# Kernel optimization log

Measured on AMD Instinct MI355X. Metric: run time of the kernel, lower is better.

## Reference

```python
import jax, jax.numpy as jnp
import numpy as np

ALPHA = 0.2  # LeakyReLU negative slope
NEG_INF = jnp.float32(-9e15)


def gat_layer(h, mask, W, a, concat):
    """Dense GAT layer (pyGAT style). h: [B,N,Fin], mask: [N,N] bool, W: [Fin,Fout], a: [2*Fout,1]."""
    Wh = h @ W                                   # [B,N,Fout]
    F_out = W.shape[-1]
    e_src = Wh @ a[:F_out]                       # [B,N,1]
    e_dst = Wh @ a[F_out:]                       # [B,N,1]
    e = jax.nn.leaky_relu(e_src + jnp.swapaxes(e_dst, -1, -2), ALPHA)  # [B,N,N]
    att = jnp.where(mask, e, NEG_INF)
    att = jax.nn.softmax(att, axis=-1)
    out = att @ Wh                               # [B,N,Fout]
    return jax.nn.elu(out) if concat else out


def setup_inputs() -> dict:
    key = jax.random.key(0)
    ks = jax.random.split(key, 8)
    B, N, nfeat, nhid, nheads, emb, nclass = 4, 2048, 128, 64, 8, 64, 16
    slices = jax.random.normal(ks[0], (B, N, nfeat), jnp.float32)
    adj = jax.random.randint(ks[1], (N, N), 0, 2, jnp.int32)
    s = 1.0 / float(np.sqrt(nfeat))
    Ws = jax.random.uniform(ks[2], (nheads, nfeat, nhid), jnp.float32, -s, s)
    As = jax.random.uniform(ks[3], (nheads, 2 * nhid, 1), jnp.float32, -s, s)
    W1 = jax.random.uniform(ks[4], (nhid * nheads, emb), jnp.float32, -s, s)
    a1 = jax.random.uniform(ks[5], (2 * emb, 1), jnp.float32, -s, s)
    W2 = jax.random.uniform(ks[6], (emb, nclass), jnp.float32, -s, s)
    a2 = jax.random.uniform(ks[7], (2 * nclass, 1), jnp.float32, -s, s)
    return {"slices": slices, "adj": adj, "Ws": Ws, "As": As,
            "W1": W1, "a1": a1, "W2": W2, "a2": a2}


def reference(slices, adj, Ws, As, W1, a1, W2, a2):
    # Eval mode: dropout = 0 (identity).
    mask = adj > 0                               # [N,N], broadcasts over batch
    # Multi-head GAT with concat=True (ELU inside each head), vectorized over heads.
    heads = jax.vmap(lambda W, a: gat_layer(slices, mask, W, a, True))(Ws, As)  # [H,B,N,nhid]
    H, B, N, nh = heads.shape
    x = jnp.moveaxis(heads, 0, 2).reshape(B, N, H * nh)  # concat along features, head-major
    image_feature = jax.nn.elu(gat_layer(x, mask, W1, a1, False))              # [B,N,emb]
    pre = jax.nn.elu(gat_layer(image_feature, mask, W2, a2, False))            # [B,N,nclass]
    pre = pre[:, 0, :]                                                         # [B,nclass]
    return image_feature, pre
```

## Files before the change

kernel.cpp:

```cpp
#include <hip/hip_runtime.h>
#include <hip/hip_bf16.h>
#include <cstdint>


#define NN 2048

typedef float f32x4 __attribute__((ext_vector_type(4)));
typedef __bf16 bf16x8 __attribute__((ext_vector_type(8)));
typedef _Float16 f16;
typedef _Float16 f16x8 __attribute__((ext_vector_type(8)));

__device__ __forceinline__ void gll16(const void* g, void* l) {
  __builtin_amdgcn_global_load_lds(
      (const __attribute__((address_space(1))) unsigned int*)g,
      (__attribute__((address_space(3))) unsigned int*)l, 16, 0, 0);
}

__global__ __launch_bounds__(256) void prep_k(
    const int* __restrict__ adj, unsigned char* __restrict__ pm,
    const float* __restrict__ Ws, __bf16* __restrict__ WsFh, __bf16* __restrict__ WsFl,
    const float* __restrict__ W1, __bf16* __restrict__ W1Fh, __bf16* __restrict__ W1Fl) {
  const int bx = blockIdx.x, t = threadIdx.x;
  if (bx < 2048) {
    const int i = bx;
#pragma unroll
    for (int jt = 0; jt < 8; ++jt) {
      const int j = jt * 256 + t;
      pm[((long)(j >> 5) << 16) + i * 32 + (j & 31)] =
          adj[(long)i * NN + j] > 0 ? 0xFFu : 0u;
    }
  } else if (bx < 2304) {
    const int idx = (bx - 2048) * 256 + t;
    const int inst = idx >> 13;
    const int rem = idx & 8191;
    const int k = rem >> 6, n = rem & 63;
    const float v = Ws[(long)inst * 8192 + rem];
    const __bf16 vh = (__bf16)v;
    const int pos = ((k >> 5) * 4 + (n >> 4)) * 512 + (((k >> 3) & 3) * 16 + (n & 15)) * 8 + (k & 7);
    WsFh[(long)inst * 8192 + pos] = vh;
    WsFl[(long)inst * 8192 + pos] = (__bf16)(v - (float)vh);
  } else {
    const int idx = (bx - 2304) * 256 + t;
    const int k = idx >> 6, n = idx & 63;
    const float v = W1[idx];
    const __bf16 vh = (__bf16)v;
    const int pos = ((k >> 5) * 4 + (n >> 4)) * 512 + (((k >> 3) & 3) * 16 + (n & 15)) * 8 + (k & 7);
    W1Fh[pos] = vh;
    W1Fl[pos] = (__bf16)(v - (float)vh);
  }
}

struct GemmLd {
  float4 a0, a1;
  bf16x8 bh[4], bl[4];
};

__global__ __launch_bounds__(128) void gemm_mfma_k(
    const float* __restrict__ Aall, const __bf16* __restrict__ WFhi,
    const __bf16* __restrict__ WFlo, const float* __restrict__ avecAll,
    f16* __restrict__ WhBAll, float* __restrict__ Eo, float* __restrict__ Go,
    f16* __restrict__ Fo, f16* __restrict__ Ho, float* __restrict__ pC,
    int K, int KS, long aStrideB) {
  const int p = blockIdx.y;
  const int ks = blockIdx.z;
  const float* A = Aall + (long)(p & 3) * aStrideB;
  const long wfOff = (long)(p >> 2) * K * 64;
  const bf16x8* BhF = (const bf16x8*)(WFhi + wfOff);
  const bf16x8* BlF = (const bf16x8*)(WFlo + wfOff);

  const int t = threadIdx.x, lane = t & 63, wave = t >> 6;
  const int quad = lane >> 4, lm = lane & 15;
  const int i0w = blockIdx.x * 32 + wave * 16;
  const float* Arow = A + (long)(i0w + lm) * K;
  const int kBeg = ks * (K / KS), kEnd = kBeg + K / KS;

  f32x4 acc[4];
#pragma unroll
  for (int nt = 0; nt < 4; ++nt) acc[nt] = (f32x4){0.f, 0.f, 0.f, 0.f};

  auto LOAD = [&](GemmLd& L, int k0) {
    L.a0 = *(const float4*)(Arow + k0 + quad * 8);
    L.a1 = *(const float4*)(Arow + k0 + quad * 8 + 4);
    const int bbase = (k0 >> 5) * 256 + lane;
#pragma unroll
    for (int nt = 0; nt < 4; ++nt) {
      L.bh[nt] = BhF[bbase + nt * 64];
      L.bl[nt] = BlF[bbase + nt * 64];
    }
  };
  auto STEP = [&](const GemmLd& L) {
    const float av8[8] = {L.a0.x, L.a0.y, L.a0.z, L.a0.w, L.a1.x, L.a1.y, L.a1.z, L.a1.w};
    bf16x8 ah, al;
#pragma unroll
    for (int j = 0; j < 8; ++j) {
      const __bf16 h = (__bf16)av8[j];
      ah[j] = h;
      al[j] = (__bf16)(av8[j] - (float)h);
    }
#pragma unroll
    for (int nt = 0; nt < 4; ++nt) {
      acc[nt] = __builtin_amdgcn_mfma_f32_16x16x32_bf16(ah, L.bh[nt], acc[nt], 0, 0, 0);
      acc[nt] = __builtin_amdgcn_mfma_f32_16x16x32_bf16(al, L.bh[nt], acc[nt], 0, 0, 0);
      acc[nt] = __builtin_amdgcn_mfma_f32_16x16x32_bf16(ah, L.bl[nt], acc[nt], 0, 0, 0);
    }
  };

  GemmLd La, Lb;
  LOAD(La, kBeg);
  for (int k0 = kBeg; k0 < kEnd; k0 += 64) {
    LOAD(Lb, k0 + 32);
    STEP(La);
    LOAD(La, (k0 + 64 < kEnd) ? k0 + 64 : kBeg);
    STEP(Lb);
  }

  if (KS > 1) {
    float* pc = pC + ((long)(p * KS + ks) * NN) * 64;
#pragma unroll
    for (int reg = 0; reg < 4; ++reg) {
      const int row = i0w + quad * 4 + reg;
#pragma unroll
      for (int nt = 0; nt < 4; ++nt) pc[(long)row * 64 + nt * 16 + lm] = acc[nt][reg];
    }
    return;
  }

  const float* av = avecAll + (long)(p >> 2) * 128;
  f16* WhB = WhBAll + (long)p * NN * 64;
  float* E = Eo + (long)p * NN;
  float* G = Go + (long)p * NN;
  f16* F = Fo + (long)p * NN;
  f16* Hh = Ho + (long)p * NN;

  float alo[4], ahi[4];
#pragma unroll
  for (int nt = 0; nt < 4; ++nt) {
    alo[nt] = av[nt * 16 + lm];
    ahi[nt] = av[64 + nt * 16 + lm];
  }
#pragma unroll
  for (int reg = 0; reg < 4; ++reg) {
    float es = 0.f, ed = 0.f;
#pragma unroll
    for (int nt = 0; nt < 4; ++nt) {
      es += acc[nt][reg] * alo[nt];
      ed += acc[nt][reg] * ahi[nt];
    }
#pragma unroll
    for (int m = 1; m < 16; m <<= 1) {
      es += __shfl_xor(es, m);
      ed += __shfl_xor(ed, m);
    }
    if (lm == 0) {
      const int r = i0w + quad * 4 + reg;
      E[r] = __expf(es);
      G[r] = __expf(0.2f * es);
      F[r] = (f16)__expf(ed);
      Hh[r] = (f16)__expf(0.2f * ed);
    }
  }

  const int r0 = i0w + quad * 4;
  const long base = ((long)(r0 >> 5) * 4) * 512 + (((r0 >> 3) & 3) * 16 + lm) * 8 + (r0 & 7);
#pragma unroll
  for (int nt = 0; nt < 4; ++nt) {
    union { f16 h[4]; uint2 u; } pk;
#pragma unroll
    for (int q = 0; q < 4; ++q) pk.h[q] = (f16)acc[nt][q];
    *(uint2*)(WhB + base + nt * 512) = pk.u;
  }
}

__global__ __launch_bounds__(256) void gemm_epi_k(
    const float* __restrict__ pC, const float* __restrict__ avec,
    f16* __restrict__ WhBAll, float* __restrict__ Eo, float* __restrict__ Go,
    f16* __restrict__ Fo, f16* __restrict__ Ho, int KS) {
  const int inst = blockIdx.y;
  const int t = threadIdx.x;
  const int row = blockIdx.x * 16 + (t >> 4);
  const int cg = t & 15;
  f32x4 c = (f32x4){0.f, 0.f, 0.f, 0.f};
  for (int ks = 0; ks < KS; ++ks)
    c += *(const f32x4*)(pC + (((long)(inst * KS + ks) * NN) + row) * 64 + cg * 4);
  float es = 0.f, ed = 0.f;
#pragma unroll
  for (int q = 0; q < 4; ++q) {
    const int n = cg * 4 + q;
    es += c[q] * avec[n];
    ed += c[q] * avec[64 + n];
  }
#pragma unroll
  for (int m = 1; m < 16; m <<= 1) {
    es += __shfl_xor(es, m);
    ed += __shfl_xor(ed, m);
  }
  if (cg == 0) {
    Eo[(long)inst * NN + row] = __expf(es);
    Go[(long)inst * NN + row] = __expf(0.2f * es);
    Fo[(long)inst * NN + row] = (f16)__expf(ed);
    Ho[(long)inst * NN + row] = (f16)__expf(0.2f * ed);
  }
  f16* WhB = WhBAll + (long)inst * NN * 64;
#pragma unroll
  for (int q = 0; q < 4; ++q) {
    const int n = cg * 4 + q;
    const int pos = ((row >> 5) * 4 + (n >> 4)) * 512 + (((row >> 3) & 3) * 16 + (n & 15)) * 8 + (row & 7);
    WhB[pos] = (f16)c[q];
  }
}

__global__ __launch_bounds__(1024, 4) void attn_k(
    const f16* __restrict__ WhBAll, const float* __restrict__ Eb,
    const float* __restrict__ Gb, const f16* __restrict__ Fb,
    const f16* __restrict__ Hb, const unsigned char* __restrict__ pm,
    float* __restrict__ out1, int rowStride, long strideB,
    int jsCount, float* __restrict__ partAcc, float* __restrict__ partSum) {
  const int p = blockIdx.z;
  const int js = blockIdx.y;
  const f16* WhB = WhBAll + (long)p * NN * 64;
  const float* E = Eb + (long)p * NN;
  const float* G = Gb + (long)p * NN;
  const f16* F = Fb + (long)p * NN;
  const f16* Hv = Hb + (long)p * NN;
  const int t = threadIdx.x, lane = t & 63, wave = t >> 6;
  const int rw = wave & 3, q = wave >> 2;
  const int quad = lane >> 4, lm = lane & 15;
  const int i0 = blockIdx.x * 128;
  const int rbase = rw * 32;
  const int span = 64 / jsCount;
  const int nIter = span / 4;
  const int kbBeg = js * span + q * nIter;

  __shared__ __align__(16) char pool[73728];
  f16* Fs = (f16*)pool;
  f16* Hs = (f16*)(pool + 4096);
  char* ring = pool + 8192 + q * 16384;

  const int r0g = i0 + rbase + lm, r1g = i0 + rbase + 16 + lm;
  const f16 e0 = (f16)E[r0g], g0 = (f16)G[r0g];
  const f16 e1 = (f16)E[r1g], g1 = (f16)G[r1g];
  f16x8 e0v, g0v, e1v, g1v;
#pragma unroll
  for (int j = 0; j < 8; ++j) { e0v[j] = e0; g0v[j] = g0; e1v[j] = e1; g1v[j] = g1; }

  f16x8 ones;
#pragma unroll
  for (int j = 0; j < 8; ++j) ones[j] = (lm == 0) ? (f16)1.0f : (f16)0.0f;

  if (wave == 0) {
#pragma unroll
    for (int c = 0; c < 4; ++c) gll16((const char*)F + c * 1024 + lane * 16, pool + c * 1024);
  } else if (wave == 1) {
#pragma unroll
    for (int c = 0; c < 4; ++c) gll16((const char*)Hv + c * 1024 + lane * 16, pool + 4096 + c * 1024);
  }
  if (rw == 0) {
    const char* gB = (const char*)WhB + (long)kbBeg * 4096;
    const unsigned char* gM = pm + ((long)kbBeg << 16) + i0 * 32;
#pragma unroll
    for (int c = 0; c < 4; ++c) gll16(gB + c * 1024 + lane * 16, ring + c * 1024);
#pragma unroll
    for (int c = 0; c < 4; ++c) gll16(gM + c * 1024 + lane * 16, ring + 4096 + c * 1024);
  }
  __syncthreads();

  f32x4 acc0[4], acc1[4], sum0, sum1;
#pragma unroll
  for (int nt = 0; nt < 4; ++nt) {
    acc0[nt] = (f32x4){0.f, 0.f, 0.f, 0.f};
    acc1[nt] = (f32x4){0.f, 0.f, 0.f, 0.f};
  }
  sum0 = (f32x4){0.f, 0.f, 0.f, 0.f};
  sum1 = (f32x4){0.f, 0.f, 0.f, 0.f};

  for (int i = 0; i < nIter; ++i) {
    const int kb = kbBeg + i;
    if (rw == 0 && i + 1 < nIter) {
      char* dst = ring + ((i + 1) & 1) * 8192;
      const char* gB = (const char*)WhB + (long)(kb + 1) * 4096;
      const unsigned char* gM = pm + ((long)(kb + 1) << 16) + i0 * 32;
#pragma unroll
      for (int c = 0; c < 4; ++c) gll16(gB + c * 1024 + lane * 16, dst + c * 1024);
#pragma unroll
      for (int c = 0; c < 4; ++c) gll16(gM + c * 1024 + lane * 16, dst + 4096 + c * 1024);
    }
    const char* slot = ring + (i & 1) * 8192;
    const f16x8 F8 = *(const f16x8*)(Fs + kb * 32 + quad * 8);
    const f16x8 H8 = *(const f16x8*)(Hs + kb * 32 + quad * 8);
    const uint2 m0 = *(const uint2*)(slot + 4096 + (rbase + lm) * 32 + quad * 8);
    const uint2 m1 = *(const uint2*)(slot + 4096 + (rbase + 16 + lm) * 32 + quad * 8);

    union { f16x8 v; uint4 u; } A0, A1;
    A0.v = __builtin_elementwise_max(e0v * F8, g0v * H8);
    A1.v = __builtin_elementwise_max(e1v * F8, g1v * H8);
    A0.u.x &= __builtin_amdgcn_perm(0u, m0.x, 0x01010000u);
    A0.u.y &= __builtin_amdgcn_perm(0u, m0.x, 0x03030202u);
    A0.u.z &= __builtin_amdgcn_perm(0u, m0.y, 0x01010000u);
    A0.u.w &= __builtin_amdgcn_perm(0u, m0.y, 0x03030202u);
    A1.u.x &= __builtin_amdgcn_perm(0u, m1.x, 0x01010000u);
    A1.u.y &= __builtin_amdgcn_perm(0u, m1.x, 0x03030202u);
    A1.u.z &= __builtin_amdgcn_perm(0u, m1.y, 0x01010000u);
    A1.u.w &= __builtin_amdgcn_perm(0u, m1.y, 0x03030202u);

#pragma unroll
    for (int nt = 0; nt < 4; ++nt) {
      const f16x8 bfr = *(const f16x8*)(slot + (nt * 64 + lane) * 16);
      acc0[nt] = __builtin_amdgcn_mfma_f32_16x16x32_f16(A0.v, bfr, acc0[nt], 0, 0, 0);
      acc1[nt] = __builtin_amdgcn_mfma_f32_16x16x32_f16(A1.v, bfr, acc1[nt], 0, 0, 0);
    }
    sum0 = __builtin_amdgcn_mfma_f32_16x16x32_f16(A0.v, ones, sum0, 0, 0, 0);
    sum1 = __builtin_amdgcn_mfma_f32_16x16x32_f16(A1.v, ones, sum1, 0, 0, 0);
    __syncthreads();
  }

  float* cmb = (float*)pool;
#pragma unroll
  for (int r = 1; r < 4; ++r) {
    if (q == r) {
      float* dst = &cmb[(rw * 64 + lane) * 40];
#pragma unroll
      for (int nt = 0; nt < 4; ++nt) {
        *(f32x4*)(dst + nt * 4) = acc0[nt];
        *(f32x4*)(dst + 16 + nt * 4) = acc1[nt];
      }
      *(f32x4*)(dst + 32) = sum0;
      *(f32x4*)(dst + 36) = sum1;
    }
    __syncthreads();
    if (q == 0) {
      const float* src = &cmb[(rw * 64 + lane) * 40];
#pragma unroll
      for (int nt = 0; nt < 4; ++nt) {
        acc0[nt] += *(const f32x4*)(src + nt * 4);
        acc1[nt] += *(const f32x4*)(src + 16 + nt * 4);
      }
      sum0 += *(const f32x4*)(src + 32);
      sum1 += *(const f32x4*)(src + 36);
    }
    if (r < 3) __syncthreads();
  }
  if (q != 0) return;

  if (jsCount == 1) {
#pragma unroll
    for (int g = 0; g < 2; ++g) {
      const f32x4* acc = g ? acc1 : acc0;
      const f32x4 sm = g ? sum1 : sum0;
#pragma unroll
      for (int reg = 0; reg < 4; ++reg) {
        const int row = i0 + rbase + g * 16 + quad * 4 + reg;
        const float ls = __shfl(sm[reg], quad * 16);
        const float il = ls > 0.f ? 1.f / ls : 0.f;
#pragma unroll
        for (int nt = 0; nt < 4; ++nt) {
          float v = acc[nt][reg] * il;
          v = v > 0.f ? v : expm1f(v);
          const long o = (long)(p & 3) * strideB + (long)row * rowStride + (p >> 2) * 64 + nt * 16 + lm;
          out1[o] = v;
        }
      }
    }
  } else {
    float* pAcc = partAcc + ((long)p * jsCount + js) * NN * 64;
    float* pSum = partSum + ((long)p * jsCount + js) * NN;
#pragma unroll
    for (int g = 0; g < 2; ++g) {
      const f32x4* acc = g ? acc1 : acc0;
      const f32x4 sm = g ? sum1 : sum0;
#pragma unroll
      for (int reg = 0; reg < 4; ++reg) {
        const int row = i0 + rbase + g * 16 + quad * 4 + reg;
#pragma unroll
        for (int nt = 0; nt < 4; ++nt) pAcc[(long)row * 64 + nt * 16 + lm] = acc[nt][reg];
        if (lm == 0) pSum[row] = sm[reg];
      }
    }
  }
}

__global__ __launch_bounds__(256) void layer3a_k(
    const float* __restrict__ partAcc, const float* __restrict__ partSum,
    const float* __restrict__ W2, const float* __restrict__ a2,
    const unsigned char* __restrict__ pm, float* __restrict__ outImg,
    float* __restrict__ pOut , int JS) {
  const int bb = blockIdx.x, chunk = blockIdx.y, t = threadIdx.x;
  __shared__ float w2alo[64], w2ahi[64];
  __shared__ float W2s[64][17];
  __shared__ float v0[64];
  __shared__ float redc[4][17];
  if (t < 64) {
    float sl = 0.f, sh = 0.f;
#pragma unroll
    for (int c = 0; c < 16; ++c) {
      const float wv = W2[t * 16 + c];
      W2s[t][c] = wv;
      sl += wv * a2[c];
      sh += wv * a2[16 + c];
    }
    w2alo[t] = sl;
    w2ahi[t] = sh;
    float s = 0.f, l0 = 0.f;
    for (int js = 0; js < JS; ++js) {
      const long b = ((long)bb * JS + js) * NN;
      s += partAcc[b * 64 + t];
      l0 += partSum[b];
    }
    float v = s * (l0 > 0.f ? 1.f / l0 : 0.f);
    v0[t] = v > 0.f ? v : expm1f(v);
  }
  __syncthreads();

  float es = 0.f;
#pragma unroll 16
  for (int k = 0; k < 64; ++k) es += v0[k] * w2alo[k];

  const int j = chunk * 256 + t;
  float arow[64];
  {
    f32x4 v[16];
#pragma unroll
    for (int qq = 0; qq < 16; ++qq) v[qq] = (f32x4){0.f, 0.f, 0.f, 0.f};
    float s = 0.f;
    for (int js = 0; js < JS; ++js) {
      const long b = ((long)bb * JS + js) * NN;
      const float* src = partAcc + (b + j) * 64;
#pragma unroll
      for (int qq = 0; qq < 16; ++qq) v[qq] += *(const f32x4*)(src + qq * 4);
      s += partSum[b + j];
    }
    const float il = s > 0.f ? 1.f / s : 0.f;
    float* orow = outImg + ((long)bb * NN + j) * 64;
#pragma unroll
    for (int qq = 0; qq < 16; ++qq) {
      f32x4 r;
#pragma unroll
      for (int u = 0; u < 4; ++u) {
        float x = v[qq][u] * il;
        r[u] = x > 0.f ? x : expm1f(x);
        arow[qq * 4 + u] = r[u];
      }
      *(f32x4*)(orow + qq * 4) = r;
    }
  }

  float ed = 0.f;
#pragma unroll
  for (int k = 0; k < 64; ++k) ed += arow[k] * w2ahi[k];
  float e = es + ed;
  e = fmaxf(e, 0.2f * e);
  const float pv = pm[((long)(j >> 5) << 16) + (j & 31)] ? __expf(e) : 0.f;

  float acc[16];
#pragma unroll
  for (int c = 0; c < 16; ++c) {
    float wh = 0.f;
#pragma unroll
    for (int k = 0; k < 64; ++k) wh += arow[k] * W2s[k][c];
    acc[c] = pv * wh;
  }
  float lsum = pv;

#pragma unroll
  for (int off = 32; off > 0; off >>= 1) {
    lsum += __shfl_down(lsum, off);
#pragma unroll
    for (int c = 0; c < 16; ++c) acc[c] += __shfl_down(acc[c], off);
  }
  if ((t & 63) == 0) {
    const int wv = t >> 6;
#pragma unroll
    for (int c = 0; c < 16; ++c) redc[wv][c] = acc[c];
    redc[wv][16] = lsum;
  }
  __syncthreads();
  if (t < 17) {
    pOut[((long)bb * 8 + chunk) * 17 + t] =
        redc[0][t] + redc[1][t] + redc[2][t] + redc[3][t];
  }
}

__global__ __launch_bounds__(64) void layer3b_k(const float* __restrict__ pOut,
                                                float* __restrict__ outPre) {
  const int t = threadIdx.x;
  if (t >= 64) return;
  const int bb = t >> 4, c = t & 15;
  float a = 0.f, l = 0.f;
#pragma unroll
  for (int ch = 0; ch < 8; ++ch) {
    a += pOut[((long)bb * 8 + ch) * 17 + c];
    l += pOut[((long)bb * 8 + ch) * 17 + 16];
  }
  float v = a / l;
  v = v > 0.f ? v : expm1f(v);
  outPre[bb * 16 + c] = v;
}

extern "C" void kernel_launch(void* const* d_in, const int* in_sizes, int n_in,
                              void* d_out, int out_size, void* d_ws, size_t ws_size,
                              hipStream_t stream) {
  (void)in_sizes; (void)n_in; (void)out_size; (void)ws_size;
  constexpr int B = 4, N = NN, JS2 = 4, KS2 = 4;

  const float* slices = (const float*)d_in[0];
  const int* adj = (const int*)d_in[1];
  const float* Ws = (const float*)d_in[2];
  const float* As = (const float*)d_in[3];
  const float* W1 = (const float*)d_in[4];
  const float* a1 = (const float*)d_in[5];
  const float* W2 = (const float*)d_in[6];
  const float* a2 = (const float*)d_in[7];
  float* out = (float*)d_out;

  char* w = (char*)d_ws;
  size_t off = 0;
  auto alloc = [&](size_t bytes) {
    void* ptr = w + off;
    off += (bytes + 255) & ~(size_t)255;
    return ptr;
  };
  unsigned char* pm = (unsigned char*)alloc((size_t)64 * 65536);
  __bf16* WsFh = (__bf16*)alloc((size_t)8 * 128 * 64 * 2);
  __bf16* WsFl = (__bf16*)alloc((size_t)8 * 128 * 64 * 2);
  __bf16* W1Fh = (__bf16*)alloc((size_t)512 * 64 * 2);
  __bf16* W1Fl = (__bf16*)alloc((size_t)512 * 64 * 2);
  f16* WhB1 = (f16*)alloc((size_t)32 * N * 64 * 2);
  float* E1 = (float*)alloc((size_t)32 * N * 4);
  float* G1 = (float*)alloc((size_t)32 * N * 4);
  f16* F1 = (f16*)alloc((size_t)32 * N * 2);
  f16* H1 = (f16*)alloc((size_t)32 * N * 2);
  float* x = (float*)alloc((size_t)B * N * 512 * 4);
  float* pC2 = (float*)alloc((size_t)B * KS2 * N * 64 * 4);
  f16* WhB2 = (f16*)alloc((size_t)B * N * 64 * 2);
  float* E2 = (float*)alloc((size_t)B * N * 4);
  float* G2 = (float*)alloc((size_t)B * N * 4);
  f16* F2 = (f16*)alloc((size_t)B * N * 2);
  f16* H2 = (f16*)alloc((size_t)B * N * 2);
  float* pAcc2 = (float*)alloc((size_t)B * JS2 * N * 64 * 4);
  float* pSum2 = (float*)alloc((size_t)B * JS2 * N * 4);
  float* pL3 = (float*)alloc((size_t)B * 8 * 17 * 4);

  prep_k<<<dim3(2432), dim3(256), 0, stream>>>(adj, pm, Ws, WsFh, WsFl, W1, W1Fh, W1Fl);

  gemm_mfma_k<<<dim3(N / 32, 32, 1), dim3(128), 0, stream>>>(
      slices, WsFh, WsFl, As, WhB1, E1, G1, F1, H1, (float*)nullptr,
      128, 1, (long)N * 128);
  attn_k<<<dim3(N / 128, 1, 32), dim3(1024), 0, stream>>>(
      WhB1, E1, G1, F1, H1, pm, x, 512, (long)N * 512,
      1, (float*)nullptr, (float*)nullptr);

  gemm_mfma_k<<<dim3(N / 32, 4, KS2), dim3(128), 0, stream>>>(
      x, W1Fh, W1Fl, a1, (f16*)nullptr, (float*)nullptr, (float*)nullptr,
      (f16*)nullptr, (f16*)nullptr, pC2, 512, KS2, (long)N * 512);
  gemm_epi_k<<<dim3(N / 16, 4), dim3(256), 0, stream>>>(
      pC2, a1, WhB2, E2, G2, F2, H2, KS2);
  attn_k<<<dim3(N / 128, JS2, 4), dim3(1024), 0, stream>>>(
      WhB2, E2, G2, F2, H2, pm, (float*)nullptr, 64, (long)N * 64,
      JS2, pAcc2, pSum2);

  layer3a_k<<<dim3(B, 8), dim3(256), 0, stream>>>(
      pAcc2, pSum2, W2, a2, pm, out, pL3, JS2);
  layer3b_k<<<dim3(1), dim3(64), 0, stream>>>(pL3, out + (size_t)B * N * 64);
}
```

Measured before the change: 182.6 us.

## Halve attention block to 512 threads, two K-steps per barrier, direct mask loads

The attention kernel now runs 8 waves split into two K-halves instead of 16 waves in four K-quarters. Each ring slot holds two key blocks, so one barrier covers two MFMA sub-steps. The adjacency mask is read straight from global memory per lane instead of staged through LDS. The cross-wave reduction collapses to a single exchange, and LDS use per block drops, which allows more resident blocks. The trade-off is less K-parallelism per block, and the mask reads are now uncoalesced 8-byte global loads on the critical path.

```diff
diff --git a/kernel.cpp b/kernel.cpp
--- a/kernel.cpp
+++ b/kernel.cpp
@@ -209,7 +209,7 @@
   }
 }
 
-__global__ __launch_bounds__(1024, 4) void attn_k(
+__global__ __launch_bounds__(512) void attn_k(
     const f16* __restrict__ WhBAll, const float* __restrict__ Eb,
     const float* __restrict__ Gb, const f16* __restrict__ Fb,
     const f16* __restrict__ Hb, const unsigned char* __restrict__ pm,
@@ -223,18 +223,19 @@
   const f16* F = Fb + (long)p * NN;
   const f16* Hv = Hb + (long)p * NN;
   const int t = threadIdx.x, lane = t & 63, wave = t >> 6;
-  const int rw = wave & 3, q = wave >> 2;
+  const int rw = wave & 3, half = wave >> 2;
   const int quad = lane >> 4, lm = lane & 15;
   const int i0 = blockIdx.x * 128;
   const int rbase = rw * 32;
   const int span = 64 / jsCount;
-  const int nIter = span / 4;
-  const int kbBeg = js * span + q * nIter;
-
-  __shared__ __align__(16) char pool[73728];
+  const int nIter = span / 2;
+  const int nStep = nIter / 2;
+  const int kbBeg = js * span + half * nIter;
+
+  __shared__ __align__(16) char pool[40960];
   f16* Fs = (f16*)pool;
   f16* Hs = (f16*)(pool + 4096);
-  char* ring = pool + 8192 + q * 16384;
+  char* ring = pool + 8192 + half * 16384;
 
   const int r0g = i0 + rbase + lm, r1g = i0 + rbase + 16 + lm;
   const f16 e0 = (f16)E[r0g], g0 = (f16)G[r0g];
@@ -256,11 +257,8 @@
   }
   if (rw == 0) {
     const char* gB = (const char*)WhB + (long)kbBeg * 4096;
-    const unsigned char* gM = pm + ((long)kbBeg << 16) + i0 * 32;
-#pragma unroll
-    for (int c = 0; c < 4; ++c) gll16(gB + c * 1024 + lane * 16, ring + c * 1024);
-#pragma unroll
-    for (int c = 0; c < 4; ++c) gll16(gM + c * 1024 + lane * 16, ring + 4096 + c * 1024);
+#pragma unroll
+    for (int c = 0; c < 8; ++c) gll16(gB + c * 1024 + lane * 16, ring + c * 1024);
   }
   __syncthreads();
 
@@ -273,73 +271,73 @@
   sum0 = (f32x4){0.f, 0.f, 0.f, 0.f};
   sum1 = (f32x4){0.f, 0.f, 0.f, 0.f};
 
-  for (int i = 0; i < nIter; ++i) {
-    const int kb = kbBeg + i;
-    if (rw == 0 && i + 1 < nIter) {
-      char* dst = ring + ((i + 1) & 1) * 8192;
-      const char* gB = (const char*)WhB + (long)(kb + 1) * 4096;
-      const unsigned char* gM = pm + ((long)(kb + 1) << 16) + i0 * 32;
-#pragma unroll
-      for (int c = 0; c < 4; ++c) gll16(gB + c * 1024 + lane * 16, dst + c * 1024);
-#pragma unroll
-      for (int c = 0; c < 4; ++c) gll16(gM + c * 1024 + lane * 16, dst + 4096 + c * 1024);
-    }
-    const char* slot = ring + (i & 1) * 8192;
-    const f16x8 F8 = *(const f16x8*)(Fs + kb * 32 + quad * 8);
-    const f16x8 H8 = *(const f16x8*)(Hs + kb * 32 + quad * 8);
-    const uint2 m0 = *(const uint2*)(slot + 4096 + (rbase + lm) * 32 + quad * 8);
-    const uint2 m1 = *(const uint2*)(slot + 4096 + (rbase + 16 + lm) * 32 + quad * 8);
-
-    union { f16x8 v; uint4 u; } A0, A1;
-    A0.v = __builtin_elementwise_max(e0v * F8, g0v * H8);
-    A1.v = __builtin_elementwise_max(e1v * F8, g1v * H8);
-    A0.u.x &= __builtin_amdgcn_perm(0u, m0.x, 0x01010000u);
-    A0.u.y &= __builtin_amdgcn_perm(0u, m0.x, 0x03030202u);
-    A0.u.z &= __builtin_amdgcn_perm(0u, m0.y, 0x01010000u);
-    A0.u.w &= __builtin_amdgcn_perm(0u, m0.y, 0x03030202u);
-    A1.u.x &= __builtin_amdgcn_perm(0u, m1.x, 0x01010000u);
-    A1.u.y &= __builtin_amdgcn_perm(0u, m1.x, 0x03030202u);
-    A1.u.z &= __builtin_amdgcn_perm(0u, m1.y, 0x01010000u);
-    A1.u.w &= __builtin_amdgcn_perm(0u, m1.y, 0x03030202u);
-
+  const unsigned char* mp0 = pm + (long)(i0 + rbase + lm) * 32 + quad * 8;
+  const unsigned char* mp1 = pm + (long)(i0 + rbase + 16 + lm) * 32 + quad * 8;
+
+  for (int s = 0; s < nStep; ++s) {
+    if (rw == 0 && s + 1 < nStep) {
+      char* dst = ring + ((s + 1) & 1) * 8192;
+      const char* gB = (const char*)WhB + (long)(kbBeg + (s + 1) * 2) * 4096;
+#pragma unroll
+      for (int c = 0; c < 8; ++c) gll16(gB + c * 1024 + lane * 16, dst + c * 1024);
+    }
+    const char* slot = ring + (s & 1) * 8192;
+#pragma unroll
+    for (int u = 0; u < 2; ++u) {
+      const int kb = kbBeg + s * 2 + u;
+      const char* bt = slot + u * 4096;
+      const uint2 m0 = *(const uint2*)(mp0 + ((long)kb << 16));
+      const uint2 m1 = *(const uint2*)(mp1 + ((long)kb << 16));
+      const f16x8 F8 = *(const f16x8*)(Fs + kb * 32 + quad * 8);
+      const f16x8 H8 = *(const f16x8*)(Hs + kb * 32 + quad * 8);
+
+      union { f16x8 v; uint4 u4; } A0, A1;
+      A0.v = __builtin_elementwise_max(e0v * F8, g0v * H8);
+      A1.v = __builtin_elementwise_max(e1v * F8, g1v * H8);
+      A0.u4.x &= __builtin_amdgcn_perm(0u, m0.x, 0x01010000u);
+      A0.u4.y &= __builtin_amdgcn_perm(0u, m0.x, 0x03030202u);
+      A0.u4.z &= __builtin_amdgcn_perm(0u, m0.y, 0x01010000u);
+      A0.u4.w &= __builtin_amdgcn_perm(0u, m0.y, 0x03030202u);
+      A1.u4.x &= __builtin_amdgcn_perm(0u, m1.x, 0x01010000u);
+      A1.u4.y &= __builtin_amdgcn_perm(0u, m1.x, 0x03030202u);
+      A1.u4.z &= __builtin_amdgcn_perm(0u, m1.y, 0x01010000u);
+      A1.u4.w &= __builtin_amdgcn_perm(0u, m1.y, 0x03030202u);
+
+#pragma unroll
+      for (int nt = 0; nt < 4; ++nt) {
+        const f16x8 bfr = *(const f16x8*)(bt + (nt * 64 + lane) * 16);
+        acc0[nt] = __builtin_amdgcn_mfma_f32_16x16x32_f16(A0.v, bfr, acc0[nt], 0, 0, 0);
+        acc1[nt] = __builtin_amdgcn_mfma_f32_16x16x32_f16(A1.v, bfr, acc1[nt], 0, 0, 0);
+      }
+      sum0 = __builtin_amdgcn_mfma_f32_16x16x32_f16(A0.v, ones, sum0, 0, 0, 0);
+      sum1 = __builtin_amdgcn_mfma_f32_16x16x32_f16(A1.v, ones, sum1, 0, 0, 0);
+    }
+    __syncthreads();
+  }
+
+  float* cmb = (float*)pool;
+  if (half == 1) {
+    float* dst = &cmb[(rw * 64 + lane) * 40];
 #pragma unroll
     for (int nt = 0; nt < 4; ++nt) {
-      const f16x8 bfr = *(const f16x8*)(slot + (nt * 64 + lane) * 16);
-      acc0[nt] = __builtin_amdgcn_mfma_f32_16x16x32_f16(A0.v, bfr, acc0[nt], 0, 0, 0);
-      acc1[nt] = __builtin_amdgcn_mfma_f32_16x16x32_f16(A1.v, bfr, acc1[nt], 0, 0, 0);
-    }
-    sum0 = __builtin_amdgcn_mfma_f32_16x16x32_f16(A0.v, ones, sum0, 0, 0, 0);
-    sum1 = __builtin_amdgcn_mfma_f32_16x16x32_f16(A1.v, ones, sum1, 0, 0, 0);
-    __syncthreads();
-  }
-
-  float* cmb = (float*)pool;
-#pragma unroll
-  for (int r = 1; r < 4; ++r) {
-    if (q == r) {
-      float* dst = &cmb[(rw * 64 + lane) * 40];
-#pragma unroll
-      for (int nt = 0; nt < 4; ++nt) {
-        *(f32x4*)(dst + nt * 4) = acc0[nt];
-        *(f32x4*)(dst + 16 + nt * 4) = acc1[nt];
-      }
-      *(f32x4*)(dst + 32) = sum0;
-      *(f32x4*)(dst + 36) = sum1;
-    }
-    __syncthreads();
-    if (q == 0) {
-      const float* src = &cmb[(rw * 64 + lane) * 40];
-#pragma unroll
-      for (int nt = 0; nt < 4; ++nt) {
-        acc0[nt] += *(const f32x4*)(src + nt * 4);
-        acc1[nt] += *(const f32x4*)(src + 16 + nt * 4);
-      }
-      sum0 += *(const f32x4*)(src + 32);
-      sum1 += *(const f32x4*)(src + 36);
-    }
-    if (r < 3) __syncthreads();
-  }
-  if (q != 0) return;
+      *(f32x4*)(dst + nt * 4) = acc0[nt];
+      *(f32x4*)(dst + 16 + nt * 4) = acc1[nt];
+    }
+    *(f32x4*)(dst + 32) = sum0;
+    *(f32x4*)(dst + 36) = sum1;
+  }
+  __syncthreads();
+  if (half == 1) return;
+  {
+    const float* src = &cmb[(rw * 64 + lane) * 40];
+#pragma unroll
+    for (int nt = 0; nt < 4; ++nt) {
+      acc0[nt] += *(const f32x4*)(src + nt * 4);
+      acc1[nt] += *(const f32x4*)(src + 16 + nt * 4);
+    }
+    sum0 += *(const f32x4*)(src + 32);
+    sum1 += *(const f32x4*)(src + 36);
+  }
 
   if (jsCount == 1) {
 #pragma unroll
@@ -544,7 +542,7 @@
   gemm_mfma_k<<<dim3(N / 32, 32, 1), dim3(128), 0, stream>>>(
       slices, WsFh, WsFl, As, WhB1, E1, G1, F1, H1, (float*)nullptr,
       128, 1, (long)N * 128);
-  attn_k<<<dim3(N / 128, 1, 32), dim3(1024), 0, stream>>>(
+  attn_k<<<dim3(N / 128, 1, 32), dim3(512), 0, stream>>>(
       WhB1, E1, G1, F1, H1, pm, x, 512, (long)N * 512,
       1, (float*)nullptr, (float*)nullptr);
 
@@ -553,7 +551,7 @@
       (f16*)nullptr, (f16*)nullptr, pC2, 512, KS2, (long)N * 512);
   gemm_epi_k<<<dim3(N / 16, 4), dim3(256), 0, stream>>>(
       pC2, a1, WhB2, E2, G2, F2, H2, KS2);
-  attn_k<<<dim3(N / 128, JS2, 4), dim3(1024), 0, stream>>>(
+  attn_k<<<dim3(N / 128, JS2, 4), dim3(512), 0, stream>>>(
       WhB2, E2, G2, F2, H2, pm, (float*)nullptr, 64, (long)N * 64,
       JS2, pAcc2, pSum2);
 
```

Result: faster. 172.2 us (-5.7%).
